# Performance work log

Hardware: AMD Instinct MI355X
Metric: run time of the kernel (lower is better)

The kernel has to match this reference:

```python
import jax, jax.numpy as jnp
import numpy as np

N_DOC, SEQ, HID, HEADS = 4, 1024, 768, 12
NE, NM, NP = 48, 4, 1000
L, EMB, BLK, GHID = 97, 768, 64, 500
NEDGE_R = 800


def setup_inputs() -> dict:
    key = jax.random.key(0)
    ks = jax.random.split(key, 24)
    s = 0.02
    att = jax.random.uniform(ks[1], (N_DOC, HEADS, SEQ, SEQ), jnp.float32)
    inp = {
        "sequence_output": jax.random.normal(ks[0], (N_DOC, SEQ, HID), jnp.float32),
        "attention": att / att.sum(-1, keepdims=True),
        "mention_starts": jax.random.randint(ks[2], (N_DOC, NE, NM), 0, SEQ - 2),
        "mention_mask": jnp.ones((N_DOC, NE, NM), jnp.bool_),
        "hts": jax.random.randint(ks[3], (N_DOC, NP, 2), 0, NE),
        "label_emb": jax.random.normal(ks[4], (L, EMB), jnp.float32),
        "gat_W0": jax.random.normal(ks[5], (EMB, 2 * GHID), jnp.float32) * s,
        "gat_al0": jax.random.normal(ks[6], (2, GHID), jnp.float32) * s,
        "gat_ar0": jax.random.normal(ks[7], (2, GHID), jnp.float32) * s,
        "gat_b0": jnp.zeros((2 * GHID,), jnp.float32),
        "gat_W1": jax.random.normal(ks[8], (2 * GHID, EMB), jnp.float32) * s,
        "gat_al1": jax.random.normal(ks[9], (1, EMB), jnp.float32) * s,
        "gat_ar1": jax.random.normal(ks[10], (1, EMB), jnp.float32) * s,
        "gat_b1": jnp.zeros((EMB,), jnp.float32),
        "edge_src": jnp.concatenate([jax.random.randint(ks[11], (NEDGE_R,), 0, L), jnp.arange(L)]),
        "edge_dst": jnp.concatenate([jax.random.randint(ks[12], (NEDGE_R,), 0, L), jnp.arange(L)]),
        "head_W": jax.random.normal(ks[13], (2 * HID, EMB), jnp.float32) * s,
        "head_b": jnp.zeros((EMB,), jnp.float32),
        "tail_W": jax.random.normal(ks[14], (2 * HID, EMB), jnp.float32) * s,
        "tail_b": jnp.zeros((EMB,), jnp.float32),
        "ln_g": jnp.ones((L,), jnp.float32),
        "ln_b": jnp.zeros((L,), jnp.float32),
        "lin2_W": jax.random.normal(ks[15], (2 * L, L), jnp.float32) * s,
        "lin2_b": jnp.zeros((L,), jnp.float32),
        "bil_W": jax.random.normal(ks[16], (EMB * BLK + L, L), jnp.float32) * s,
        "bil_b": jnp.zeros((L,), jnp.float32),
    }
    return inp


def gat_layer(x, W, al, ar, b, src, dst, n_nodes):
    # DGL-style GATConv: per-head linear, additive attention, softmax over incoming edges.
    heads, out_dim = al.shape
    feat = (x @ W).reshape(-1, heads, out_dim)          # [N, H, D]
    el = (feat * al[None]).sum(-1)                      # [N, H]
    er = (feat * ar[None]).sum(-1)
    e = jax.nn.leaky_relu(el[src] + er[dst], 0.2)       # [E, H]
    emax = jax.ops.segment_max(e, dst, num_segments=n_nodes)
    w = jnp.exp(e - emax[dst])
    den = jax.ops.segment_sum(w, dst, num_segments=n_nodes)
    alpha = w / (den[dst] + 1e-9)
    out = jax.ops.segment_sum(alpha[:, :, None] * feat[src], dst, num_segments=n_nodes)
    return out + b.reshape(heads, out_dim)              # [N, H, D]


def reference(sequence_output, attention, mention_starts, mention_mask, hts, label_emb,
              gat_W0, gat_al0, gat_ar0, gat_b0, gat_W1, gat_al1, gat_ar1, gat_b1,
              edge_src, edge_dst, head_W, head_b, tail_W, tail_b,
              ln_g, ln_b, lin2_W, lin2_b, bil_W, bil_b):
    n, c, d = sequence_output.shape
    nl = label_emb.shape[0]
    OFFSET = 1  # bert-style cls offset
    pos = mention_starts + OFFSET                               # [n, E, M], all < c
    bi = jnp.arange(n)[:, None, None]
    m_emb = sequence_output[bi, pos]                            # [n, E, M, d]
    m_att = attention[bi, :, pos]                               # [n, E, M, h, c]
    mf = mention_mask.astype(sequence_output.dtype)
    cnt = mf.sum(2)                                             # [n, E]
    lse = jax.nn.logsumexp(jnp.where(mention_mask[..., None], m_emb, -1e30), axis=2)
    ent_emb = jnp.where(cnt[..., None] > 0, lse, 0.0)           # [n, E, d]
    ent_att = (m_att * mf[..., None, None]).sum(2) / (cnt[..., None, None] + 1e-9)  # [n, E, h, c]
    bi2 = jnp.arange(n)[:, None]
    hidx, tidx = hts[..., 0], hts[..., 1]
    hs = ent_emb[bi2, hidx]                                     # [n, P, d]
    ts = ent_emb[bi2, tidx]
    ht = (ent_att[bi2, hidx] * ent_att[bi2, tidx]).mean(2)      # [n, P, c]
    ht = ht / (ht.sum(-1, keepdims=True) + 1e-5)
    rs = jnp.einsum('npc,ncd->npd', ht, sequence_output)        # [n, P, d]
    hs, ts, rs = hs.reshape(-1, d), ts.reshape(-1, d), rs.reshape(-1, d)
    # GAT over the label co-occurrence graph
    h0 = jax.nn.elu(gat_layer(label_emb, gat_W0, gat_al0, gat_ar0, gat_b0, edge_src, edge_dst, nl))
    h0 = h0.reshape(nl, -1)                                     # concat 2 heads -> [L, 1000]
    lab = gat_layer(h0, gat_W1, gat_al1, gat_ar1, gat_b1, edge_src, edge_dst, nl).mean(1)  # [L, emb]
    def lnorm(x):
        mu = x.mean(-1, keepdims=True)
        v = ((x - mu) ** 2).mean(-1, keepdims=True)
        return (x - mu) / jnp.sqrt(v + 1e-5) * ln_g + ln_b
    hsl = lnorm(hs @ lab.T)
    tsl = lnorm(ts @ lab.T)
    logits_lab = jnp.concatenate([hsl, tsl], 1) @ lin2_W + lin2_b   # [N, L]
    h2 = jnp.tanh(jnp.concatenate([hs, rs], 1) @ head_W + head_b)   # [N, emb]
    t2 = jnp.tanh(jnp.concatenate([ts, rs], 1) @ tail_W + tail_b)
    emb = h2.shape[1]
    b1 = h2.reshape(-1, emb // BLK, BLK)
    b2 = t2.reshape(-1, emb // BLK, BLK)
    bl = (b1[:, :, :, None] * b2[:, :, None, :]).reshape(-1, emb * BLK)  # [N, emb*blk]
    logits = jnp.concatenate([bl, logits_lab], 1) @ bil_W + bil_b        # [N, L]
    return logits
```

## Files before the change

### kernel.cpp

```cpp
#include <hip/hip_runtime.h>
#include <hip/hip_bf16.h>
#include <math.h>

#define NDOC 4
#define SEQL 1024
#define HIDD 768
#define NHEADS 12
#define NEENT 48
#define NMEN 4
#define NPAIR 1000
#define NLAB 97
#define GHID 500
#define NEDGE 897
#define NROW (NDOC*NPAIR)

#define KBIL 49152
#define KSTEPS_MAIN 1536
#define KSTEPS_TOT 1540
#define NPAD 128
#define NPOUT 112
#define NCHUNK 12

#define PB_WPREP 3080
#define PB_SEQ   1536
#define PB_EMB   192
#define PB_ATT   2304

typedef __attribute__((ext_vector_type(8))) short short8v;
typedef __attribute__((ext_vector_type(4))) short short4v;
typedef __attribute__((ext_vector_type(4))) float f32x4;
typedef _Float16 half8v __attribute__((ext_vector_type(8)));
typedef _Float16 half2v __attribute__((ext_vector_type(2)));
typedef unsigned int uint4v __attribute__((ext_vector_type(4)));

__device__ __forceinline__ unsigned short f2bfbits(float x) {
    return __builtin_bit_cast(unsigned short, __float2bfloat16(x));
}

__device__ __forceinline__ float block_reduce_sum(float v, float* red) {
    int tid = threadIdx.x;
    red[tid] = v;
    __syncthreads();
    for (int s = blockDim.x >> 1; s > 0; s >>= 1) {
        if (tid < s) red[tid] += red[tid + s];
        __syncthreads();
    }
    float r = red[0];
    __syncthreads();
    return r;
}

__device__ __forceinline__ float block_reduce_max(float v, float* red) {
    int tid = threadIdx.x;
    red[tid] = v;
    __syncthreads();
    for (int s = blockDim.x >> 1; s > 0; s >>= 1) {
        if (tid < s) red[tid] = fmaxf(red[tid], red[tid + s]);
        __syncthreads();
    }
    float r = red[0];
    __syncthreads();
    return r;
}

__global__ void __launch_bounds__(256) k_prep_all(
    const float* __restrict__ bil_W, _Float16* __restrict__ Wb,
    const float* __restrict__ seq, __hip_bfloat16* __restrict__ seqb,
    const int* __restrict__ mstarts, float* __restrict__ ent_emb,
    const float* __restrict__ att, float* __restrict__ ent_att)
{
    int bid = blockIdx.x;
    if (bid < PB_WPREP) {
        int t = bid * 256 + threadIdx.x;
        int lane = t & 63;
        int nt = (t >> 6) & 7;
        int kt = t >> 9;
        int col = nt * 16 + (lane & 15);
        int kbase = kt * 32 + ((lane >> 4) << 3);
        half8v v;
        #pragma unroll
        for (int e = 0; e < 8; ++e) {
            int k = kbase + e;
            float x = (col < NLAB && k < (KBIL + NLAB)) ? bil_W[(size_t)k * NLAB + col] : 0.f;
            v[e] = (_Float16)x;
        }
        ((half8v*)Wb)[t] = v;
    } else if (bid < PB_WPREP + PB_SEQ) {
        int t = (bid - PB_WPREP) * 256 + threadIdx.x;
        int lane = t & 63;
        int rest = t >> 6;
        int dt = rest % 48; rest /= 48;
        int kt = rest % 32;
        int doc = rest / 32;
        int d = dt * 16 + (lane & 15);
        int kbase = kt * 32 + ((lane >> 4) << 3);
        short8v v;
        #pragma unroll
        for (int e = 0; e < 8; ++e)
            v[e] = (short)f2bfbits(seq[((size_t)doc * SEQL + kbase + e) * HIDD + d]);
        ((short8v*)seqb)[t] = v;
    } else if (bid < PB_WPREP + PB_SEQ + PB_EMB) {
        int be = bid - (PB_WPREP + PB_SEQ);
        int b = be / NEENT;
        int pos[NMEN];
        #pragma unroll
        for (int m = 0; m < NMEN; ++m) pos[m] = mstarts[be * NMEN + m] + 1;
        for (int d = threadIdx.x; d < HIDD; d += 256) {
            float v0 = seq[((size_t)b * SEQL + pos[0]) * HIDD + d];
            float v1 = seq[((size_t)b * SEQL + pos[1]) * HIDD + d];
            float v2 = seq[((size_t)b * SEQL + pos[2]) * HIDD + d];
            float v3 = seq[((size_t)b * SEQL + pos[3]) * HIDD + d];
            float mx = fmaxf(fmaxf(v0, v1), fmaxf(v2, v3));
            float s = expf(v0 - mx) + expf(v1 - mx) + expf(v2 - mx) + expf(v3 - mx);
            ent_emb[(size_t)be * HIDD + d] = mx + logf(s);
        }
    } else {
        int idx = bid - (PB_WPREP + PB_SEQ + PB_EMB);
        int h = idx % NHEADS;
        int be = idx / NHEADS;
        int b = be / NEENT;
        int pos[NMEN];
        #pragma unroll
        for (int m = 0; m < NMEN; ++m) pos[m] = mstarts[be * NMEN + m] + 1;
        const float* abase = att + ((size_t)b * NHEADS + h) * SEQL * SEQL;
        for (int s = threadIdx.x; s < SEQL; s += 256) {
            float acc = 0.f;
            #pragma unroll
            for (int m = 0; m < NMEN; ++m) acc += abase[(size_t)pos[m] * SEQL + s];
            ent_att[(size_t)idx * SEQL + s] = acc * 0.25f;
        }
    }
}

__global__ void __launch_bounds__(256) k_prep2(
    const float* __restrict__ head_W, __hip_bfloat16* __restrict__ Whb,
    const float* __restrict__ tail_W, __hip_bfloat16* __restrict__ Wtb,
    const float* __restrict__ ent_emb, __hip_bfloat16* __restrict__ emb_bf)
{
    int bid = blockIdx.x;
    if (bid < 1152) {
        const float* W = bid < 576 ? head_W : tail_W;
        __hip_bfloat16* Wf = bid < 576 ? Whb : Wtb;
        int t = (bid % 576) * 256 + threadIdx.x;
        int lane = t & 63;
        int ntile = (t >> 6) % 48;
        int kt = t / (48 * 64);
        int col = ntile * 16 + (lane & 15);
        int kbase = kt * 32 + ((lane >> 4) << 3);
        short8v v;
        #pragma unroll
        for (int e = 0; e < 8; ++e)
            v[e] = (short)f2bfbits(W[(size_t)(kbase + e) * HIDD + col]);
        ((short8v*)Wf)[t] = v;
    } else {
        int t = (bid - 1152) * 256 + threadIdx.x;
        if (t >= NDOC * NEENT * HIDD / 8) return;
        const float4* p = (const float4*)(ent_emb + (size_t)t * 8);
        float4 a = p[0], b = p[1];
        short8v v;
        v[0] = (short)f2bfbits(a.x); v[1] = (short)f2bfbits(a.y);
        v[2] = (short)f2bfbits(a.z); v[3] = (short)f2bfbits(a.w);
        v[4] = (short)f2bfbits(b.x); v[5] = (short)f2bfbits(b.y);
        v[6] = (short)f2bfbits(b.z); v[7] = (short)f2bfbits(b.w);
        ((short8v*)emb_bf)[t] = v;
    }
}

template<int K, int N>
__global__ void __launch_bounds__(256) k_gemm2(
    const float* __restrict__ A, const float* __restrict__ W, float* __restrict__ C)
{
    const int JT = (N + 255) / 256;
    int n  = blockIdx.x / JT;
    int jt = blockIdx.x % JT;
    int j = jt * 256 + threadIdx.x;
    if (j >= N) return;
    const float* a = A + (size_t)n * K;
    float acc0 = 0.f, acc1 = 0.f, acc2 = 0.f, acc3 = 0.f;
    float acc4 = 0.f, acc5 = 0.f, acc6 = 0.f, acc7 = 0.f;
    for (int k = 0; k < K; k += 8) {
        acc0 += a[k + 0] * W[(size_t)(k + 0) * N + j];
        acc1 += a[k + 1] * W[(size_t)(k + 1) * N + j];
        acc2 += a[k + 2] * W[(size_t)(k + 2) * N + j];
        acc3 += a[k + 3] * W[(size_t)(k + 3) * N + j];
        acc4 += a[k + 4] * W[(size_t)(k + 4) * N + j];
        acc5 += a[k + 5] * W[(size_t)(k + 5) * N + j];
        acc6 += a[k + 6] * W[(size_t)(k + 6) * N + j];
        acc7 += a[k + 7] * W[(size_t)(k + 7) * N + j];
    }
    C[(size_t)n * N + j] = ((acc0 + acc1) + (acc2 + acc3)) + ((acc4 + acc5) + (acc6 + acc7));
}

template<int NH, int OD>
__global__ void k_eler(const float* __restrict__ feat, const float* __restrict__ al,
                       const float* __restrict__ ar, float* __restrict__ el,
                       float* __restrict__ er)
{
    __shared__ float red[256];
    int n = blockIdx.x;
    for (int h = 0; h < NH; ++h) {
        float a = 0.f, b = 0.f;
        for (int k = threadIdx.x; k < OD; k += blockDim.x) {
            float f = feat[(size_t)n * NH * OD + h * OD + k];
            a += f * al[h * OD + k];
            b += f * ar[h * OD + k];
        }
        float sa = block_reduce_sum(a, red);
        float sb = block_reduce_sum(b, red);
        if (threadIdx.x == 0) { el[n * NH + h] = sa; er[n * NH + h] = sb; }
    }
}

template<int NH, int OD, int QN, int DO_ELU>
__global__ void k_gat_agg(const float* __restrict__ feat,
                          const float* __restrict__ el, const float* __restrict__ er,
                          const int* __restrict__ esrc, const int* __restrict__ edst,
                          const float* __restrict__ bias, float* __restrict__ out)
{
    __shared__ float red[256];
    __shared__ int ss[NEDGE];
    __shared__ int dd[NEDGE];
    int n = blockIdx.x;
    for (int t = threadIdx.x; t < NEDGE; t += blockDim.x) { ss[t] = esrc[t]; dd[t] = edst[t]; }
    __syncthreads();
    float ern[NH], emax[NH], den[NH];
    #pragma unroll
    for (int h = 0; h < NH; ++h) ern[h] = er[n * NH + h];
    #pragma unroll
    for (int h = 0; h < NH; ++h) {
        float mx = -1e30f;
        for (int t = threadIdx.x; t < NEDGE; t += blockDim.x) {
            if (dd[t] == n) {
                float x = el[ss[t] * NH + h] + ern[h];
                x = x > 0.f ? x : 0.2f * x;
                mx = fmaxf(mx, x);
            }
        }
        emax[h] = block_reduce_max(mx, red);
        float sm = 0.f;
        for (int t = threadIdx.x; t < NEDGE; t += blockDim.x) {
            if (dd[t] == n) {
                float x = el[ss[t] * NH + h] + ern[h];
                x = x > 0.f ? x : 0.2f * x;
                sm += expf(x - emax[h]);
            }
        }
        den[h] = block_reduce_sum(sm, red);
    }
    float acc[QN];
    #pragma unroll
    for (int q = 0; q < QN; ++q) acc[q] = 0.f;
    for (int t = 0; t < NEDGE; ++t) {
        if (dd[t] != n) continue;
        int s = ss[t];
        float alpha[NH];
        #pragma unroll
        for (int h = 0; h < NH; ++h) {
            float x = el[s * NH + h] + ern[h];
            x = x > 0.f ? x : 0.2f * x;
            alpha[h] = expf(x - emax[h]) / (den[h] + 1e-9f);
        }
        #pragma unroll
        for (int q = 0; q < QN; ++q) {
            int idx = threadIdx.x + q * 256;
            if (idx < NH * OD) {
                int h = idx / OD;
                acc[q] += alpha[h] * feat[(size_t)s * NH * OD + idx];
            }
        }
    }
    #pragma unroll
    for (int q = 0; q < QN; ++q) {
        int idx = threadIdx.x + q * 256;
        if (idx < NH * OD) {
            float v = acc[q] + bias[idx];
            out[(size_t)n * NH * OD + idx] = DO_ELU ? (v > 0.f ? v : expm1f(v)) : v;
        }
    }
}

__global__ void k_labtrans(const float* __restrict__ lab, float* __restrict__ labT)
{
    int t = blockIdx.x * 256 + threadIdx.x;
    if (t >= NLAB * HIDD) return;
    int l = t / HIDD, d = t - l * HIDD;
    labT[d * NLAB + l] = lab[t];
}

__global__ void __launch_bounds__(128) k_ent_lab(
    const float* __restrict__ ent_emb, const float* __restrict__ labT,
    const float* __restrict__ ln_g, const float* __restrict__ ln_b,
    float* __restrict__ EL)
{
    __shared__ float e[HIDD];
    __shared__ float red[128];
    int be = blockIdx.x;
    for (int k = threadIdx.x; k < HIDD; k += 128) e[k] = ent_emb[(size_t)be * HIDD + k];
    __syncthreads();
    int l = threadIdx.x;
    float a = 0.f;
    if (l < NLAB)
        for (int k = 0; k < HIDD; ++k) a += e[k] * labT[k * NLAB + l];
    float v = (l < NLAB) ? a : 0.f;
    float s  = block_reduce_sum(v, red);
    float s2 = block_reduce_sum(v * v, red);
    const float invL = 1.0f / NLAB;
    float mu = s * invL;
    float var = s2 * invL - mu * mu;
    float is = 1.0f / sqrtf(var + 1e-5f);
    if (l < NLAB) EL[be * NLAB + l] = (a - mu) * is * ln_g[l] + ln_b[l];
}

__global__ void __launch_bounds__(128) k_lin2(
    const float* __restrict__ EL, const int* __restrict__ hts,
    const float* __restrict__ lin2_W, const float* __restrict__ lin2_b,
    _Float16* __restrict__ llhf)
{
    __shared__ float sh[NLAB], st[NLAB];
    int n = blockIdx.x;
    int b = n / NPAIR;
    int hi = hts[n * 2], ti = hts[n * 2 + 1];
    int l = threadIdx.x;
    if (l < NLAB) {
        sh[l] = EL[(b * NEENT + hi) * NLAB + l];
        st[l] = EL[(b * NEENT + ti) * NLAB + l];
    }
    __syncthreads();
    float a = 0.f;
    if (l < NLAB) {
        a = lin2_b[l];
        for (int q = 0; q < NLAB; ++q)
            a += sh[q] * lin2_W[q * NLAB + l] + st[q] * lin2_W[(NLAB + q) * NLAB + l];
    }
    llhf[(size_t)n * NPAD + l] = (_Float16)(l < NLAB ? a : 0.f);
}

__global__ void __launch_bounds__(256) k_ht(
    const float* __restrict__ ent_att, const int* __restrict__ hts,
    __hip_bfloat16* __restrict__ HTb)
{
    __shared__ float red[256];
    int n = blockIdx.x;
    n = (n & 7) * 500 + (n >> 3);
    int b = n / NPAIR;
    int hi = hts[n * 2], ti = hts[n * 2 + 1];
    const float* ha = ent_att + ((size_t)(b * NEENT + hi)) * NHEADS * SEQL;
    const float* ta = ent_att + ((size_t)(b * NEENT + ti)) * NHEADS * SEQL;
    int s0 = threadIdx.x * 4;
    float4 acc = {0.f, 0.f, 0.f, 0.f};
    #pragma unroll
    for (int h = 0; h < NHEADS; ++h) {
        float4 a = *(const float4*)&ha[h * SEQL + s0];
        float4 t = *(const float4*)&ta[h * SEQL + s0];
        acc.x += a.x * t.x; acc.y += a.y * t.y; acc.z += a.z * t.z; acc.w += a.w * t.w;
    }
    const float inv12 = 1.0f / NHEADS;
    acc.x *= inv12; acc.y *= inv12; acc.z *= inv12; acc.w *= inv12;
    float Z = block_reduce_sum(acc.x + acc.y + acc.z + acc.w, red);
    float scale = 1.0f / (Z + 1e-5f);
    int nloc = n % NPAIR;
    short4v v;
    v.x = (short)f2bfbits(acc.x * scale);
    v.y = (short)f2bfbits(acc.y * scale);
    v.z = (short)f2bfbits(acc.z * scale);
    v.w = (short)f2bfbits(acc.w * scale);
    *(short4v*)&HTb[((size_t)b * 1024 + nloc) * SEQL + s0] = v;
}

__global__ void __launch_bounds__(256) k_rs_mfma(
    const __hip_bfloat16* __restrict__ HTb, const __hip_bfloat16* __restrict__ seqb,
    __hip_bfloat16* __restrict__ rsb)
{
    int b = blockIdx.x;
    int wg = (b & 7) * 96 + (b >> 3);
    int doc = wg / 192;
    int rem = wg % 192;
    int mtile = rem / 6, ngrp = rem % 6;
    int tid = threadIdx.x, wave = tid >> 6, lane = tid & 63;
    int mh = wave & 1, ng = wave >> 1;
    int lr = lane & 15, lg = lane >> 4;
    int rowl = mtile * 32 + mh * 16 + lr;
    const short8v* av = (const short8v*)(HTb + (((size_t)doc * 1024 + rowl) * SEQL));
    const short8v* bv = (const short8v*)seqb;
    int dtbase = ngrp * 8 + ng * 4;
    f32x4 acc[4];
    #pragma unroll
    for (int nt = 0; nt < 4; ++nt) acc[nt] = f32x4{0.f, 0.f, 0.f, 0.f};
    for (int kt = 0; kt < 32; ++kt) {
        short8v af = av[kt * 4 + lg];
        const short8v* wp = bv + ((((size_t)doc * 32 + kt) * 48 + dtbase) * 64 + lane);
        #pragma unroll
        for (int nt = 0; nt < 4; ++nt)
            acc[nt] = __builtin_amdgcn_mfma_f32_16x16x32_bf16(af, wp[nt * 64], acc[nt], 0, 0, 0);
    }
    #pragma unroll
    for (int nt = 0; nt < 4; ++nt) {
        int d = ngrp * 128 + ng * 64 + nt * 16 + lr;
        #pragma unroll
        for (int r = 0; r < 4; ++r) {
            int nloc = mtile * 32 + mh * 16 + lg * 4 + r;
            if (nloc < NPAIR)
                rsb[((size_t)(doc * NPAIR + nloc)) * HIDD + d] = __float2bfloat16(acc[nt][r]);
        }
    }
}

__global__ void __launch_bounds__(256) k_ht2_mfma(
    const __hip_bfloat16* __restrict__ emb_bf, const __hip_bfloat16* __restrict__ rsb,
    const int* __restrict__ hts,
    const __hip_bfloat16* __restrict__ Whb, const __hip_bfloat16* __restrict__ Wtb,
    const float* __restrict__ head_b, const float* __restrict__ tail_b,
    float* __restrict__ h2, float* __restrict__ t2)
{
    int bid = blockIdx.x;
    int which = bid >= 750 ? 1 : 0;
    int rem = bid - which * 750;
    int mtile = rem / 6, ngrp = rem % 6;
    int tid = threadIdx.x, wave = tid >> 6, lane = tid & 63;
    int mh = wave & 1, ng = wave >> 1;
    int lr = lane & 15, lg = lane >> 4;
    int n = mtile * 32 + mh * 16 + lr;
    int b = n / NPAIR;
    int ent = hts[n * 2 + which];
    const short8v* embrow = (const short8v*)emb_bf + (size_t)(b * NEENT + ent) * 96;
    const short8v* rsrow  = (const short8v*)rsb + (size_t)n * 96;
    const short8v* wv = (const short8v*)(which ? Wtb : Whb);
    const float* bias = which ? tail_b : head_b;
    float* out = which ? t2 : h2;
    f32x4 acc[4];
    #pragma unroll
    for (int nt = 0; nt < 4; ++nt) acc[nt] = f32x4{0.f, 0.f, 0.f, 0.f};
    int ntbase = ngrp * 8 + ng * 4;
    for (int kt = 0; kt < 24; ++kt) {
        short8v af = embrow[kt * 4 + lg];
        const short8v* wp = wv + ((kt * 48 + ntbase) * 64 + lane);
        #pragma unroll
        for (int nt = 0; nt < 4; ++nt)
            acc[nt] = __builtin_amdgcn_mfma_f32_16x16x32_bf16(af, wp[nt * 64], acc[nt], 0, 0, 0);
    }
    for (int kt = 24; kt < 48; ++kt) {
        short8v af = rsrow[(kt - 24) * 4 + lg];
        const short8v* wp = wv + ((kt * 48 + ntbase) * 64 + lane);
        #pragma unroll
        for (int nt = 0; nt < 4; ++nt)
            acc[nt] = __builtin_amdgcn_mfma_f32_16x16x32_bf16(af, wp[nt * 64], acc[nt], 0, 0, 0);
    }
    #pragma unroll
    for (int nt = 0; nt < 4; ++nt) {
        int col = ngrp * 128 + ng * 64 + nt * 16 + lr;
        float bj = bias[col];
        #pragma unroll
        for (int r = 0; r < 4; ++r) {
            int n2 = mtile * 32 + mh * 16 + lg * 4 + r;
            out[(size_t)n2 * HIDD + col] = tanhf(acc[nt][r] + bj);
        }
    }
}

__global__ void __launch_bounds__(256) k_bilin_mfma(
    const float* __restrict__ h2, const float* __restrict__ t2,
    const _Float16* __restrict__ llhf, const _Float16* __restrict__ Wb,
    float* __restrict__ pout)
{
    __shared__ unsigned int hs2[32 * 68];
    __shared__ _Float16 ts[32 * 72];
    int bid = blockIdx.x;
    int c = bid % NCHUNK;
    int mtile = bid / NCHUNK;
    int n0 = mtile * 32;
    int tid = threadIdx.x;
    int wave = tid >> 6, lane = tid & 63;
    int mh = wave & 1, ng = wave >> 1;
    int lr = lane & 15;
    int lg = lane >> 4;
    int koff = lg << 3;
    int row = mh * 16 + lr;
    f32x4 acc[4];
    #pragma unroll
    for (int nt = 0; nt < 4; ++nt) acc[nt] = f32x4{0.f, 0.f, 0.f, 0.f};

    const half8v* wbv = (const half8v*)Wb;

    for (int idx = tid; idx < 2048; idx += 256) {
        int r = idx >> 6, cc = idx & 63;
        float hv = h2[(size_t)(n0 + r) * HIDD + c * 64 + cc];
        float tv = t2[(size_t)(n0 + r) * HIDD + c * 64 + cc];
        unsigned short hb = __builtin_bit_cast(unsigned short, (_Float16)hv);
        hs2[r * 68 + cc] = ((unsigned int)hb << 16) | hb;
        ts[r * 72 + cc] = (_Float16)tv;
    }
    __syncthreads();
    for (int j0 = 0; j0 < 64; j0 += 32) {
        half8v tv8 = *(const half8v*)&ts[row * 72 + j0 + koff];
        int ktbase = c * 128 + (j0 >> 5);
        #pragma unroll 4
        for (int i = 0; i < 64; ++i) {
            unsigned int hh = hs2[row * 68 + i];
            half8v hbc = __builtin_bit_cast(half8v, uint4v{hh, hh, hh, hh});
            half8v af = hbc * tv8;
            int kt = ktbase + i * 2;
            const half8v* wp = wbv + ((kt * 8 + ng * 4) * 64 + lane);
            #pragma unroll
            for (int nt = 0; nt < 4; ++nt) {
                half8v bf = wp[nt * 64];
                acc[nt] = __builtin_amdgcn_mfma_f32_16x16x32_f16(af, bf, acc[nt], 0, 0, 0);
            }
        }
    }
    if (c == NCHUNK - 1) {
        const half8v* lv = (const half8v*)llhf;
        #pragma unroll
        for (int tt = 0; tt < 4; ++tt) {
            half8v af = lv[(size_t)(n0 + row) * 16 + tt * 4 + lg];
            int kt = KSTEPS_MAIN + tt;
            const half8v* wp = wbv + ((kt * 8 + ng * 4) * 64 + lane);
            #pragma unroll
            for (int nt = 0; nt < 4; ++nt)
                acc[nt] = __builtin_amdgcn_mfma_f32_16x16x32_f16(af, wp[nt * 64], acc[nt], 0, 0, 0);
        }
    }
    #pragma unroll
    for (int nt = 0; nt < 4; ++nt) {
        int col = ng * 64 + nt * 16 + lr;
        if (col < NPOUT) {
            #pragma unroll
            for (int r = 0; r < 4; ++r) {
                int rown = n0 + mh * 16 + lg * 4 + r;
                pout[((size_t)c * NROW + rown) * NPOUT + col] = acc[nt][r];
            }
        }
    }
}

__global__ void k_bilin_reduce(const float* __restrict__ pout,
                               const float* __restrict__ bil_b,
                               float* __restrict__ out)
{
    int t = blockIdx.x * 256 + threadIdx.x;
    if (t >= NROW * NLAB) return;
    int n = t / NLAB, l = t - n * NLAB;
    float a = bil_b[l];
    #pragma unroll
    for (int q = 0; q < NCHUNK; ++q) a += pout[((size_t)q * NROW + n) * NPOUT + l];
    out[t] = a;
}

extern "C" void kernel_launch(void* const* d_in, const int* in_sizes, int n_in,
                              void* d_out, int out_size, void* d_ws, size_t ws_size,
                              hipStream_t stream)
{
    (void)in_sizes; (void)n_in; (void)out_size; (void)ws_size;
    const float* seq       = (const float*)d_in[0];
    const float* att       = (const float*)d_in[1];
    const int*   mstarts   = (const int*)d_in[2];
    const int*   hts       = (const int*)d_in[4];
    const float* label_emb = (const float*)d_in[5];
    const float* gat_W0    = (const float*)d_in[6];
    const float* gat_al0   = (const float*)d_in[7];
    const float* gat_ar0   = (const float*)d_in[8];
    const float* gat_b0    = (const float*)d_in[9];
    const float* gat_W1    = (const float*)d_in[10];
    const float* gat_al1   = (const float*)d_in[11];
    const float* gat_ar1   = (const float*)d_in[12];
    const float* gat_b1    = (const float*)d_in[13];
    const int*   esrc      = (const int*)d_in[14];
    const int*   edst      = (const int*)d_in[15];
    const float* head_W    = (const float*)d_in[16];
    const float* head_b    = (const float*)d_in[17];
    const float* tail_W    = (const float*)d_in[18];
    const float* tail_b    = (const float*)d_in[19];
    const float* ln_g      = (const float*)d_in[20];
    const float* ln_b      = (const float*)d_in[21];
    const float* lin2_W    = (const float*)d_in[22];
    const float* lin2_b    = (const float*)d_in[23];
    const float* bil_W     = (const float*)d_in[24];
    const float* bil_b     = (const float*)d_in[25];
    float* out = (float*)d_out;
    float* ws  = (float*)d_ws;

    float* ent_emb    = ws;
    float* ent_att    = ws + 147456;
    float* rs_region  = ws + 2506752;
    float* h2         = ws + 5578752;
    float* t2         = ws + 8650752;
    float* EL         = ws + 11722752;
    float* labT       = ws + 11741376;
    float* feat0      = ws + 12110752;
    float* el0        = ws + 12207752;
    float* er0        = ws + 12207952;
    float* h0         = ws + 12208152;
    float* feat1      = ws + 12305152;
    float* el1        = ws + 12379648;
    float* er1        = ws + 12379752;
    float* lab        = ws + 12379856;
    _Float16* llhf    = (_Float16*)(ws + 12454352);
    _Float16* Wb      = (_Float16*)(ws + 12710352);
    __hip_bfloat16* Whb    = (__hip_bfloat16*)(ws + 147456);
    __hip_bfloat16* Wtb    = (__hip_bfloat16*)(ws + 147456 + 589824);
    __hip_bfloat16* emb_bf = (__hip_bfloat16*)(ws + 147456 + 1179648);
    float* pout = ws + 147456;
    __hip_bfloat16* HTb  = (__hip_bfloat16*)h2;
    __hip_bfloat16* seqb = (__hip_bfloat16*)t2;
    __hip_bfloat16* rsb  = (__hip_bfloat16*)rs_region;

    k_prep_all<<<PB_WPREP + PB_SEQ + PB_EMB + PB_ATT, 256, 0, stream>>>(
        bil_W, Wb, seq, seqb, mstarts, ent_emb, att, ent_att);

    k_gemm2<768, 1000><<<NLAB * 4, 256, 0, stream>>>(label_emb, gat_W0, feat0);
    k_eler<2, 500><<<NLAB, 256, 0, stream>>>(feat0, gat_al0, gat_ar0, el0, er0);
    k_gat_agg<2, 500, 4, 1><<<NLAB, 256, 0, stream>>>(feat0, el0, er0, esrc, edst, gat_b0, h0);
    k_gemm2<1000, 768><<<NLAB * 3, 256, 0, stream>>>(h0, gat_W1, feat1);
    k_eler<1, 768><<<NLAB, 256, 0, stream>>>(feat1, gat_al1, gat_ar1, el1, er1);
    k_gat_agg<1, 768, 3, 0><<<NLAB, 256, 0, stream>>>(feat1, el1, er1, esrc, edst, gat_b1, lab);

    k_labtrans<<<(NLAB * HIDD + 255) / 256, 256, 0, stream>>>(lab, labT);
    k_ent_lab<<<NDOC * NEENT, 128, 0, stream>>>(ent_emb, labT, ln_g, ln_b, EL);
    k_lin2<<<NROW, 128, 0, stream>>>(EL, hts, lin2_W, lin2_b, llhf);

    k_ht<<<NROW, 256, 0, stream>>>(ent_att, hts, HTb);

    k_prep2<<<1224, 256, 0, stream>>>(head_W, Whb, tail_W, Wtb, ent_emb, emb_bf);

    k_rs_mfma<<<768, 256, 0, stream>>>(HTb, seqb, rsb);

    k_ht2_mfma<<<1500, 256, 0, stream>>>(emb_bf, rsb, hts, Whb, Wtb, head_b, tail_b, h2, t2);

    k_bilin_mfma<<<1500, 256, 0, stream>>>(h2, t2, llhf, Wb, pout);
    k_bilin_reduce<<<(NROW * NLAB + 255) / 256, 256, 0, stream>>>(pout, bil_b, out);
}
```

Baseline: 522.8 us.

## Double M-tile to 64 rows in head/tail and bilinear MFMA kernels

In the head/tail projection and bilinear MFMA kernels, each wave now computes two 16-row M subtiles that share every weight (B) fragment. The block tile grows from 32 to 64 rows and the grids shrink to match. This roughly halves the weight traffic per output row, which is the main global/L2 load in the bilinear GEMM. In exchange it uses more accumulator registers and doubles LDS for the bilinear staging. The last tile also reads h2/t2/llhf rows past NROW; only the stores are masked, not those loads.

Result: faster. 470.4 us (-10.0%).

```diff
diff --git a/kernel.cpp b/kernel.cpp
--- a/kernel.cpp
+++ b/kernel.cpp
@@ -20,6 +20,7 @@
 #define NPAD 128
 #define NPOUT 112
 #define NCHUNK 12
+#define NMT64 63
 
 #define PB_WPREP 3080
 #define PB_SEQ   1536
@@ -30,7 +31,6 @@
 typedef __attribute__((ext_vector_type(4))) short short4v;
 typedef __attribute__((ext_vector_type(4))) float f32x4;
 typedef _Float16 half8v __attribute__((ext_vector_type(8)));
-typedef _Float16 half2v __attribute__((ext_vector_type(2)));
 typedef unsigned int uint4v __attribute__((ext_vector_type(4)));
 
 __device__ __forceinline__ unsigned short f2bfbits(float x) {
@@ -413,46 +413,66 @@
     float* __restrict__ h2, float* __restrict__ t2)
 {
     int bid = blockIdx.x;
-    int which = bid >= 750 ? 1 : 0;
-    int rem = bid - which * 750;
+    int which = bid >= (NMT64 * 6) ? 1 : 0;
+    int rem = bid - which * (NMT64 * 6);
     int mtile = rem / 6, ngrp = rem % 6;
     int tid = threadIdx.x, wave = tid >> 6, lane = tid & 63;
-    int mh = wave & 1, ng = wave >> 1;
+    int ng = wave & 1, mp = wave >> 1;
     int lr = lane & 15, lg = lane >> 4;
-    int n = mtile * 32 + mh * 16 + lr;
-    int b = n / NPAIR;
-    int ent = hts[n * 2 + which];
-    const short8v* embrow = (const short8v*)emb_bf + (size_t)(b * NEENT + ent) * 96;
-    const short8v* rsrow  = (const short8v*)rsb + (size_t)n * 96;
+    int na = mtile * 64 + mp * 32 + lr;
+    int nb = na + 16;
+    int nac = na < NROW ? na : NROW - 1;
+    int nbc = nb < NROW ? nb : NROW - 1;
+    int ba = nac / NPAIR, bb = nbc / NPAIR;
+    int enta = hts[nac * 2 + which];
+    int entb = hts[nbc * 2 + which];
+    const short8v* embrow_a = (const short8v*)emb_bf + (size_t)(ba * NEENT + enta) * 96;
+    const short8v* embrow_b = (const short8v*)emb_bf + (size_t)(bb * NEENT + entb) * 96;
+    const short8v* rsrow_a  = (const short8v*)rsb + (size_t)nac * 96;
+    const short8v* rsrow_b  = (const short8v*)rsb + (size_t)nbc * 96;
     const short8v* wv = (const short8v*)(which ? Wtb : Whb);
     const float* bias = which ? tail_b : head_b;
     float* out = which ? t2 : h2;
-    f32x4 acc[4];
-    #pragma unroll
-    for (int nt = 0; nt < 4; ++nt) acc[nt] = f32x4{0.f, 0.f, 0.f, 0.f};
+    f32x4 acc[2][4];
+    #pragma unroll
+    for (int m = 0; m < 2; ++m)
+        #pragma unroll
+        for (int nt = 0; nt < 4; ++nt) acc[m][nt] = f32x4{0.f, 0.f, 0.f, 0.f};
     int ntbase = ngrp * 8 + ng * 4;
     for (int kt = 0; kt < 24; ++kt) {
-        short8v af = embrow[kt * 4 + lg];
+        short8v afa = embrow_a[kt * 4 + lg];
+        short8v afb = embrow_b[kt * 4 + lg];
         const short8v* wp = wv + ((kt * 48 + ntbase) * 64 + lane);
         #pragma unroll
-        for (int nt = 0; nt < 4; ++nt)
-            acc[nt] = __builtin_amdgcn_mfma_f32_16x16x32_bf16(af, wp[nt * 64], acc[nt], 0, 0, 0);
+        for (int nt = 0; nt < 4; ++nt) {
+            short8v bf = wp[nt * 64];
+            acc[0][nt] = __builtin_amdgcn_mfma_f32_16x16x32_bf16(afa, bf, acc[0][nt], 0, 0, 0);
+            acc[1][nt] = __builtin_amdgcn_mfma_f32_16x16x32_bf16(afb, bf, acc[1][nt], 0, 0, 0);
+        }
     }
     for (int kt = 24; kt < 48; ++kt) {
-        short8v af = rsrow[(kt - 24) * 4 + lg];
+        short8v afa = rsrow_a[(kt - 24) * 4 + lg];
+        short8v afb = rsrow_b[(kt - 24) * 4 + lg];
         const short8v* wp = wv + ((kt * 48 + ntbase) * 64 + lane);
         #pragma unroll
-        for (int nt = 0; nt < 4; ++nt)
-            acc[nt] = __builtin_amdgcn_mfma_f32_16x16x32_bf16(af, wp[nt * 64], acc[nt], 0, 0, 0);
-    }
-    #pragma unroll
-    for (int nt = 0; nt < 4; ++nt) {
-        int col = ngrp * 128 + ng * 64 + nt * 16 + lr;
-        float bj = bias[col];
-        #pragma unroll
-        for (int r = 0; r < 4; ++r) {
-            int n2 = mtile * 32 + mh * 16 + lg * 4 + r;
-            out[(size_t)n2 * HIDD + col] = tanhf(acc[nt][r] + bj);
+        for (int nt = 0; nt < 4; ++nt) {
+            short8v bf = wp[nt * 64];
+            acc[0][nt] = __builtin_amdgcn_mfma_f32_16x16x32_bf16(afa, bf, acc[0][nt], 0, 0, 0);
+            acc[1][nt] = __builtin_amdgcn_mfma_f32_16x16x32_bf16(afb, bf, acc[1][nt], 0, 0, 0);
+        }
+    }
+    #pragma unroll
+    for (int m = 0; m < 2; ++m) {
+        #pragma unroll
+        for (int nt = 0; nt < 4; ++nt) {
+            int col = ngrp * 128 + ng * 64 + nt * 16 + lr;
+            float bj = bias[col];
+            #pragma unroll
+            for (int r = 0; r < 4; ++r) {
+                int n2 = mtile * 64 + mp * 32 + m * 16 + lg * 4 + r;
+                if (n2 < NROW)
+                    out[(size_t)n2 * HIDD + col] = tanhf(acc[m][nt][r] + bj);
+            }
         }
     }
 }
@@ -462,26 +482,29 @@
     const _Float16* __restrict__ llhf, const _Float16* __restrict__ Wb,
     float* __restrict__ pout)
 {
-    __shared__ unsigned int hs2[32 * 68];
-    __shared__ _Float16 ts[32 * 72];
+    __shared__ unsigned int hs2[64 * 68];
+    __shared__ _Float16 ts[64 * 72];
     int bid = blockIdx.x;
     int c = bid % NCHUNK;
     int mtile = bid / NCHUNK;
-    int n0 = mtile * 32;
+    int n0 = mtile * 64;
     int tid = threadIdx.x;
     int wave = tid >> 6, lane = tid & 63;
-    int mh = wave & 1, ng = wave >> 1;
+    int ng = wave & 1, mp = wave >> 1;
     int lr = lane & 15;
     int lg = lane >> 4;
     int koff = lg << 3;
-    int row = mh * 16 + lr;
-    f32x4 acc[4];
-    #pragma unroll
-    for (int nt = 0; nt < 4; ++nt) acc[nt] = f32x4{0.f, 0.f, 0.f, 0.f};
+    int rowa = mp * 32 + lr;
+    int rowb = rowa + 16;
+    f32x4 acc[2][4];
+    #pragma unroll
+    for (int m = 0; m < 2; ++m)
+        #pragma unroll
+        for (int nt = 0; nt < 4; ++nt) acc[m][nt] = f32x4{0.f, 0.f, 0.f, 0.f};
 
     const half8v* wbv = (const half8v*)Wb;
 
-    for (int idx = tid; idx < 2048; idx += 256) {
+    for (int idx = tid; idx < 4096; idx += 256) {
         int r = idx >> 6, cc = idx & 63;
         float hv = h2[(size_t)(n0 + r) * HIDD + c * 64 + cc];
         float tv = t2[(size_t)(n0 + r) * HIDD + c * 64 + cc];
@@ -491,19 +514,22 @@
     }
     __syncthreads();
     for (int j0 = 0; j0 < 64; j0 += 32) {
-        half8v tv8 = *(const half8v*)&ts[row * 72 + j0 + koff];
+        half8v tva = *(const half8v*)&ts[rowa * 72 + j0 + koff];
+        half8v tvb = *(const half8v*)&ts[rowb * 72 + j0 + koff];
         int ktbase = c * 128 + (j0 >> 5);
         #pragma unroll 4
         for (int i = 0; i < 64; ++i) {
-            unsigned int hh = hs2[row * 68 + i];
-            half8v hbc = __builtin_bit_cast(half8v, uint4v{hh, hh, hh, hh});
-            half8v af = hbc * tv8;
+            unsigned int ha = hs2[rowa * 68 + i];
+            unsigned int hb = hs2[rowb * 68 + i];
+            half8v afa = __builtin_bit_cast(half8v, uint4v{ha, ha, ha, ha}) * tva;
+            half8v afb = __builtin_bit_cast(half8v, uint4v{hb, hb, hb, hb}) * tvb;
             int kt = ktbase + i * 2;
             const half8v* wp = wbv + ((kt * 8 + ng * 4) * 64 + lane);
             #pragma unroll
             for (int nt = 0; nt < 4; ++nt) {
                 half8v bf = wp[nt * 64];
-                acc[nt] = __builtin_amdgcn_mfma_f32_16x16x32_f16(af, bf, acc[nt], 0, 0, 0);
+                acc[0][nt] = __builtin_amdgcn_mfma_f32_16x16x32_f16(afa, bf, acc[0][nt], 0, 0, 0);
+                acc[1][nt] = __builtin_amdgcn_mfma_f32_16x16x32_f16(afb, bf, acc[1][nt], 0, 0, 0);
             }
         }
     }
@@ -511,22 +537,30 @@
         const half8v* lv = (const half8v*)llhf;
         #pragma unroll
         for (int tt = 0; tt < 4; ++tt) {
-            half8v af = lv[(size_t)(n0 + row) * 16 + tt * 4 + lg];
+            half8v afa = lv[(size_t)(n0 + rowa) * 16 + tt * 4 + lg];
+            half8v afb = lv[(size_t)(n0 + rowb) * 16 + tt * 4 + lg];
             int kt = KSTEPS_MAIN + tt;
             const half8v* wp = wbv + ((kt * 8 + ng * 4) * 64 + lane);
             #pragma unroll
-            for (int nt = 0; nt < 4; ++nt)
-                acc[nt] = __builtin_amdgcn_mfma_f32_16x16x32_f16(af, wp[nt * 64], acc[nt], 0, 0, 0);
-        }
-    }
-    #pragma unroll
-    for (int nt = 0; nt < 4; ++nt) {
-        int col = ng * 64 + nt * 16 + lr;
-        if (col < NPOUT) {
-            #pragma unroll
-            for (int r = 0; r < 4; ++r) {
-                int rown = n0 + mh * 16 + lg * 4 + r;
-                pout[((size_t)c * NROW + rown) * NPOUT + col] = acc[nt][r];
+            for (int nt = 0; nt < 4; ++nt) {
+                half8v bf = wp[nt * 64];
+                acc[0][nt] = __builtin_amdgcn_mfma_f32_16x16x32_f16(afa, bf, acc[0][nt], 0, 0, 0);
+                acc[1][nt] = __builtin_amdgcn_mfma_f32_16x16x32_f16(afb, bf, acc[1][nt], 0, 0, 0);
+            }
+        }
+    }
+    #pragma unroll
+    for (int m = 0; m < 2; ++m) {
+        #pragma unroll
+        for (int nt = 0; nt < 4; ++nt) {
+            int col = ng * 64 + nt * 16 + lr;
+            if (col < NPOUT) {
+                #pragma unroll
+                for (int r = 0; r < 4; ++r) {
+                    int rown = n0 + mp * 32 + m * 16 + lg * 4 + r;
+                    if (rown < NROW)
+                        pout[((size_t)c * NROW + rown) * NPOUT + col] = acc[m][nt][r];
+                }
             }
         }
     }
@@ -623,8 +657,8 @@
 
     k_rs_mfma<<<768, 256, 0, stream>>>(HTb, seqb, rsb);
 
-    k_ht2_mfma<<<1500, 256, 0, stream>>>(emb_bf, rsb, hts, Whb, Wtb, head_b, tail_b, h2, t2);
-
-    k_bilin_mfma<<<1500, 256, 0, stream>>>(h2, t2, llhf, Wb, pout);
+    k_ht2_mfma<<<2 * NMT64 * 6, 256, 0, stream>>>(emb_bf, rsb, hts, Whb, Wtb, head_b, tail_b, h2, t2);
+
+    k_bilin_mfma<<<NMT64 * NCHUNK, 256, 0, stream>>>(h2, t2, llhf, Wb, pout);
     k_bilin_reduce<<<(NROW * NLAB + 255) / 256, 256, 0, stream>>>(pout, bil_b, out);
 }
```
